# Kernel optimization log

Hardware: AMD Instinct MI355X
Metric: run time of the kernel (lower is better)

Reference implementation:

```python
import jax, jax.numpy as jnp
from jax import lax
import numpy as np

N_VOX = 50000
B = 2
D, H, W = 8, 160, 160
CIN = 16
G = 3
K = 27
CHANS = [(16, 16), (16, 32), (32, 64), (64, 64), (64, 128)]
NAMES = ['in', 'e1', 'e2', 'e3', 'out']


def setup_inputs() -> dict:
    key = jax.random.key(0)
    ks = jax.random.split(key, 16)
    rng = np.random.default_rng(0)
    # unique active cells -> deterministic scatter/gather rulebook
    lin = rng.choice(B * D * H * W, size=N_VOX, replace=False)
    bz = lin // (D * H * W)
    rem = lin % (D * H * W)
    zz = rem // (H * W)
    yy = (rem % (H * W)) // W
    xx = rem % W
    coors = jnp.asarray(np.stack([bz, zz, yy, xx], 1).astype(np.int32))
    inp = {
        'voxel_features': jax.random.normal(ks[0], (N_VOX, CIN), jnp.float32),
        'coors': coors,
        'batch_size': B,
    }
    i = 1
    for nm, (ci, co) in zip(NAMES, CHANS):
        k1, k2 = jax.random.split(ks[i]); i += 1
        inp['wb_' + nm] = jax.random.normal(k1, (K, ci, co), jnp.float32) * 0.05
        inp['ws_' + nm] = jax.random.normal(k2, (K, ci, G, co), jnp.float32) * 0.05
        inp['gm_' + nm] = jnp.ones((co,), jnp.float32)
        inp['bt_' + nm] = jnp.zeros((co,), jnp.float32)
    return inp


def _kan_block(feat, nbr, wb, ws, gm, bt, centers, inv_h):
    # submanifold KAN conv: gather -> (silu base + RBF spline basis) GEMM -> accumulate
    n = feat.shape[0]
    fp = jnp.concatenate([feat, jnp.zeros((1, feat.shape[1]), feat.dtype)], 0)  # pad row for out-of-grid

    def body(acc, kin):
        idx, wbk, wsk = kin
        x = fp[idx]                                   # [N, Cin] gathered neighbors
        base = jax.nn.silu(x) @ wbk                   # [N, Cout]
        bas = jnp.exp(-jnp.square((x[:, :, None] - centers) * inv_h))  # [N, Cin, G]
        spl = jnp.einsum('ncg,cgo->no', bas, wsk)     # [N, Cout]
        return acc + base + spl, None

    out0 = jnp.zeros((n, wb.shape[-1]), feat.dtype)
    out, _ = lax.scan(jax.checkpoint(body), out0, (nbr, wb, ws))
    # BatchNorm1d (train-mode batch stats) + ReLU
    mu = out.mean(0)
    var = out.var(0)
    out = (out - mu) * lax.rsqrt(var + 1e-3) * gm + bt
    return jax.nn.relu(out)


def _build_rulebook(coors, batch_size, n):
    grid = jnp.full((batch_size, D + 2, H + 2, W + 2), n, jnp.int32)
    grid = grid.at[coors[:, 0], coors[:, 1] + 1, coors[:, 2] + 1, coors[:, 3] + 1].set(
        jnp.arange(n, dtype=jnp.int32))
    offs = [(dz, dy, dx) for dz in (-1, 0, 1) for dy in (-1, 0, 1) for dx in (-1, 0, 1)]
    return jnp.stack([
        grid[coors[:, 0], coors[:, 1] + 1 + dz, coors[:, 2] + 1 + dy, coors[:, 3] + 1 + dx]
        for dz, dy, dx in offs])  # [27, N]


def reference(voxel_features, coors, batch_size,
              wb_in, ws_in, gm_in, bt_in,
              wb_e1, ws_e1, gm_e1, bt_e1,
              wb_e2, ws_e2, gm_e2, bt_e2,
              wb_e3, ws_e3, gm_e3, bt_e3,
              wb_out, ws_out, gm_out, bt_out):
    n = voxel_features.shape[0]
    nbr = _build_rulebook(coors, batch_size, n)
    centers = jnp.linspace(-1.0, 1.0, G)
    inv_h = (G - 1) / 2.0
    x = _kan_block(voxel_features, nbr, wb_in, ws_in, gm_in, bt_in, centers, inv_h)
    x = _kan_block(x, nbr, wb_e1, ws_e1, gm_e1, bt_e1, centers, inv_h)
    x = _kan_block(x, nbr, wb_e2, ws_e2, gm_e2, bt_e2, centers, inv_h)
    x = _kan_block(x, nbr, wb_e3, ws_e3, gm_e3, bt_e3, centers, inv_h)
    x = _kan_block(x, nbr, wb_out, ws_out, gm_out, bt_out, centers, inv_h)
    co = x.shape[1]
    dense = jnp.zeros((batch_size, D, H, W, co), x.dtype)
    dense = dense.at[coors[:, 0], coors[:, 1], coors[:, 2], coors[:, 3]].set(x)
    dense = dense.transpose(0, 4, 1, 2, 3)            # [B, C, D, H, W]
    return dense.reshape(batch_size, co * D, H, W)    # [B, C*D, H, W]
```

## Files before the change

### kernel.cpp

```cpp
#include <hip/hip_runtime.h>

#define N_VOX 50000
#define BATCH 2
#define DD 8
#define HH 160
#define WW 160
#define PD 10
#define PH 162
#define PW 162
#define KK 27
#define NCELL (BATCH*DD*HH*WW)
#define GRID_ELEMS (BATCH*PD*PH*PW)
#define OUT_ELEMS (BATCH*128*DD*HH*WW)

typedef __attribute__((ext_vector_type(8))) short short8v;
typedef __attribute__((ext_vector_type(4))) float float4v;

__device__ inline unsigned short f2bf(float f) {
    unsigned u = __float_as_uint(f);
    u += 0x7FFFu + ((u >> 16) & 1u);
    return (unsigned short)(u >> 16);
}

__device__ inline void gload_lds16(const void* g, void* l) {
    __builtin_amdgcn_global_load_lds(
        (const __attribute__((address_space(1))) void*)g,
        (__attribute__((address_space(3))) void*)l, 16, 0, 0);
}

__global__ void k_flags(const int* __restrict__ coors, int* __restrict__ flags) {
    int n = blockIdx.x * 256 + threadIdx.x;
    if (n >= N_VOX) return;
    int b = coors[n*4+0], z = coors[n*4+1], y = coors[n*4+2], x = coors[n*4+3];
    flags[((b*DD + z)*HH + y)*WW + x] = 1;
}

__global__ void k_scan1(const int* __restrict__ flags, int* __restrict__ scanout,
                        int* __restrict__ bsums) {
    __shared__ int s[256];
    int t = threadIdx.x, blk = blockIdx.x;
    int4 v = ((const int4*)(flags + blk*1024))[t];
    int tsum = v.x + v.y + v.z + v.w;
    s[t] = tsum; __syncthreads();
    for (int off = 1; off < 256; off <<= 1) {
        int x = (t >= off) ? s[t-off] : 0;
        __syncthreads(); s[t] += x; __syncthreads();
    }
    int excl = s[t] - tsum;
    int4 o; o.x = excl; o.y = excl + v.x; o.z = o.y + v.y; o.w = o.z + v.z;
    ((int4*)(scanout + blk*1024))[t] = o;
    if (t == 255) bsums[blk] = s[255];
}

__global__ void k_scan2(int* __restrict__ bsums) {
    __shared__ int s[512];
    int t = threadIdx.x;
    int orig = (t < 400) ? bsums[t] : 0;
    s[t] = orig; __syncthreads();
    for (int off = 1; off < 512; off <<= 1) {
        int x = (t >= off) ? s[t-off] : 0;
        __syncthreads(); s[t] += x; __syncthreads();
    }
    if (t < 400) bsums[t] = s[t] - orig;
}

__global__ void k_pos(const int* __restrict__ coors, const int* __restrict__ scanout,
                      const int* __restrict__ bsums, int* __restrict__ pos_of,
                      int* __restrict__ vox_at) {
    int n = blockIdx.x * 256 + threadIdx.x;
    if (n >= N_VOX) return;
    int b = coors[n*4+0], z = coors[n*4+1], y = coors[n*4+2], x = coors[n*4+3];
    int lin = ((b*DD + z)*HH + y)*WW + x;
    int pos = scanout[lin] + bsums[lin >> 10];
    pos_of[n] = pos;
    vox_at[pos] = n;
}

__global__ void k_gridP(const int* __restrict__ coors, const int* __restrict__ pos_of,
                        int* __restrict__ gridP) {
    int n = blockIdx.x * 256 + threadIdx.x;
    if (n >= N_VOX) return;
    int b = coors[n*4+0], z = coors[n*4+1], y = coors[n*4+2], x = coors[n*4+3];
    gridP[((b*PD + z+1)*PH + (y+1))*PW + (x+1)] = pos_of[n];
}

__global__ void k_nbrP(const int* __restrict__ coors, const int* __restrict__ vox_at,
                       const int* __restrict__ gridP, int* __restrict__ nbrP) {
    int i = blockIdx.x * 256 + threadIdx.x;
    if (i >= N_VOX) return;
    int n = vox_at[i];
    int b = coors[n*4+0], z = coors[n*4+1]+1, y = coors[n*4+2]+1, x = coors[n*4+3]+1;
    int k = 0;
    for (int dz = -1; dz <= 1; ++dz)
        for (int dy = -1; dy <= 1; ++dy)
            for (int dx = -1; dx <= 1; ++dx) {
                int g = gridP[((b*PD + z+dz)*PH + (y+dy))*PW + (x+dx)];
                nbrP[k*N_VOX + i] = (g >= 0) ? g : N_VOX;
                ++k;
            }
}

__global__ void k_phi0(const float* __restrict__ vf, const int* __restrict__ vox_at,
                       unsigned short* __restrict__ phi) {
    int e = blockIdx.x * 256 + threadIdx.x;
    if (e >= (N_VOX + 1) * 16) return;
    int i = e / 16, c = e % 16;
    float x = 0.f;
    if (i < N_VOX) x = vf[(size_t)vox_at[i] * 16 + c];
    float sig = 1.f / (1.f + __expf(-x));
    ushort4 p;
    p.x = f2bf(x * sig);
    p.y = f2bf(__expf(-(x + 1.f) * (x + 1.f)));
    p.z = f2bf(__expf(-x * x));
    p.w = f2bf(__expf(-(x - 1.f) * (x - 1.f)));
    *(ushort4*)&phi[(size_t)e * 4] = p;
}

struct WswzArgs {
    const float* wb[5];
    const float* ws[5];
    unsigned short* dst[5];
};
__global__ void k_wswz_all(WswzArgs a) {
    constexpr int off[6]   = {0, 27648, 82944, 304128, 746496, 1631232};
    constexpr int lgCI4[5] = {6, 6, 7, 8, 8};
    constexpr int lgCO[5]  = {4, 5, 6, 6, 7};
    int e = blockIdx.x * 256 + threadIdx.x;
    if (e >= off[5]) return;
    int L = 0;
    #pragma unroll
    for (int i = 1; i < 5; ++i) L += (e >= off[i]);
    int el = e - off[L];
    int CIN4 = 1 << lgCI4[L], COUT = 1 << lgCO[L], CIN = CIN4 >> 2;
    int j8   = el & 7;
    int rest = el >> 3;
    int o    = rest & (COUT - 1);
    int kb   = rest >> lgCO[L];
    int kabs = kb * 8 + j8;
    int k  = kabs >> lgCI4[L];
    int c4 = kabs & (CIN4 - 1);
    int c = c4 >> 2, jj = c4 & 3;
    float v = (jj == 0) ? a.wb[L][(k * CIN + c) * COUT + o]
                        : a.ws[L][((k * CIN + c) * 3 + (jj - 1)) * COUT + o];
    a.dst[L][el] = f2bf(v);
}

template<int CIN, int COUT, int NSPL>
__global__ __launch_bounds__(64, 2) void k_conv_mfma(
    const unsigned short* __restrict__ phi,
    const int*            __restrict__ nbrP,
    const unsigned short* __restrict__ Wsw,
    float*                __restrict__ pre,
    float*                __restrict__ sums)
{
    constexpr int CIN4   = CIN * 4;
    constexpr int BK     = 64;
    constexpr int SPK    = CIN4 / BK;
    constexpr int NSTAGE = KK * SPK;
    constexpr int COUTH  = COUT / NSPL;
    constexpr int NFW    = COUTH / 16;
    constexpr int WR     = 4;
    constexpr int NMB    = (N_VOX + 63) / 64;
    constexpr int NBLK   = NMB * NSPL;
    constexpr int PERX   = (NBLK + 7) / 8;

    int lb = blockIdx.x;
    int linear = (lb & 7) * PERX + (lb >> 3);
    if (linear >= NBLK) return;
    const int mb = linear / NSPL, h = linear % NSPL;

    const int lane = threadIdx.x & 63;
    const int l15 = lane & 15, q = lane >> 4;
    const int base = mb * 64;
    int vg[WR];
    #pragma unroll
    for (int rs = 0; rs < WR; ++rs) vg[rs] = base + rs * 16 + l15;
    const int ob = h * COUTH;

    const unsigned short* bp = Wsw + (size_t)(q * COUT + ob + l15) * 8;

    int rows[WR], rowsN[WR];
    short8v A0[2][WR], A1[2][WR];
    short8v B0[2][NFW], B1[2][NFW];

    auto loadB = [&](int sp, short8v (&Bb)[2][NFW]) {
        #pragma unroll
        for (int kk = 0; kk < 2; ++kk)
            #pragma unroll
            for (int nf = 0; nf < NFW; ++nf)
                Bb[kk][nf] = *(const short8v*)(bp +
                    ((size_t)(sp * 8 + kk * 4) * COUT + nf * 16) * 8);
    };
    auto loadA = [&](int sp, short8v (&Ab)[2][WR]) {
        if (sp % SPK == 0) {
            #pragma unroll
            for (int rs = 0; rs < WR; ++rs) rows[rs] = rowsN[rs];
        }
        const int c4s = (sp % SPK) * BK;
        #pragma unroll
        for (int rs = 0; rs < WR; ++rs) {
            const unsigned short* p = phi + (size_t)rows[rs] * CIN4 + c4s + q * 8;
            Ab[0][rs] = *(const short8v*)p;
            Ab[1][rs] = *(const short8v*)(p + 32);
        }
        if (sp % SPK == 0) {
            int k2 = sp / SPK + 1;
            if (k2 < KK) {
                #pragma unroll
                for (int rs = 0; rs < WR; ++rs)
                    rowsN[rs] = (vg[rs] < N_VOX) ? nbrP[k2 * N_VOX + vg[rs]] : N_VOX;
            }
        }
    };

    float4v acc[WR][NFW];
    #pragma unroll
    for (int rs = 0; rs < WR; ++rs)
        #pragma unroll
        for (int nf = 0; nf < NFW; ++nf)
            acc[rs][nf] = (float4v){0.f, 0.f, 0.f, 0.f};

    auto domfma = [&](const short8v (&Ab)[2][WR], const short8v (&Bb)[2][NFW]) {
        #pragma unroll
        for (int kk = 0; kk < 2; ++kk)
            #pragma unroll
            for (int nf = 0; nf < NFW; ++nf)
                #pragma unroll
                for (int rs = 0; rs < WR; ++rs)
                    acc[rs][nf] = __builtin_amdgcn_mfma_f32_16x16x32_bf16(
                        Ab[kk][rs], Bb[kk][nf], acc[rs][nf], 0, 0, 0);
    };

    #pragma unroll
    for (int rs = 0; rs < WR; ++rs) {
        rows[rs]  = (vg[rs] < N_VOX) ? nbrP[vg[rs]] : N_VOX;
        rowsN[rs] = (vg[rs] < N_VOX) ? nbrP[N_VOX + vg[rs]] : N_VOX;
    }
    loadB(0, B0);
    #pragma unroll
    for (int rs = 0; rs < WR; ++rs) {
        const unsigned short* p = phi + (size_t)rows[rs] * CIN4 + q * 8;
        A0[0][rs] = *(const short8v*)p;
        A0[1][rs] = *(const short8v*)(p + 32);
    }

    #define SLOT(T, Ac, Bc, An, Bn)                                   \
        if ((T) + 1 < NSTAGE) { loadB((T) + 1, Bn); loadA((T) + 1, An); } \
        __builtin_amdgcn_sched_barrier(0);                            \
        domfma(Ac, Bc);

    int s = 0;
    for (; s + 2 <= NSTAGE; s += 2) {
        SLOT(s + 0, A0, B0, A1, B1)
        SLOT(s + 1, A1, B1, A0, B0)
    }
    if constexpr (NSTAGE % 2 != 0) {
        domfma(A0, B0);
    }
    #undef SLOT

    #pragma unroll
    for (int rs = 0; rs < WR; ++rs)
        #pragma unroll
        for (int nf = 0; nf < NFW; ++nf)
            #pragma unroll
            for (int r = 0; r < 4; ++r) {
                int v = base + rs * 16 + q * 4 + r;
                if (v < N_VOX)
                    pre[(size_t)v * COUT + ob + nf * 16 + l15] = acc[rs][nf][r];
            }

    float* S = sums + (blockIdx.x & 7) * 256;
    #pragma unroll
    for (int nf = 0; nf < NFW; ++nf) {
        float s1 = 0.f, s2 = 0.f;
        #pragma unroll
        for (int rs = 0; rs < WR; ++rs)
            #pragma unroll
            for (int r = 0; r < 4; ++r) {
                int v = base + rs * 16 + q * 4 + r;
                if (v < N_VOX) {
                    float a = acc[rs][nf][r];
                    s1 += a; s2 += a * a;
                }
            }
        s1 += __shfl_xor(s1, 16); s1 += __shfl_xor(s1, 32);
        s2 += __shfl_xor(s2, 16); s2 += __shfl_xor(s2, 32);
        if (q == 0) {
            atomicAdd(&S[ob + nf * 16 + l15], s1);
            atomicAdd(&S[COUT + ob + nf * 16 + l15], s2);
        }
    }
}

template<int CIN, int COUT, int NSPL>
__global__ __launch_bounds__(256, 2) void k_conv_bsh(
    const unsigned short* __restrict__ phi,
    const int*            __restrict__ nbrP,
    const unsigned short* __restrict__ Wsw,
    float*                __restrict__ pre,
    float*                __restrict__ sums)
{
    constexpr int CIN4   = CIN * 4;
    constexpr int BK     = 64;
    constexpr int SPK    = CIN4 / BK;
    constexpr int NSTAGE = KK * SPK;
    constexpr int KB_G   = 8 * SPK;
    constexpr int COUTH  = COUT / NSPL;
    constexpr int NFW    = COUTH / 16;
    constexpr int WR     = 2;
    constexpr int NMB    = (N_VOX + 127) / 128;
    constexpr int NBLK   = NMB * NSPL;
    constexpr int PERX   = (NBLK + 7) / 8;
    constexpr int SI     = 2 * SPK;
    constexpr int VMCG   = 4 * SPK + 2;

    __shared__ short8v ldsB[2][KB_G][64];

    int lb = blockIdx.x;
    int linear = (lb & 7) * PERX + (lb >> 3);
    if (linear >= NBLK) return;
    const int mb = linear / NSPL, h = linear % NSPL;

    const int t = threadIdx.x, lane = t & 63, w = t >> 6;
    const int l15 = lane & 15, q = lane >> 4;
    const int base = mb * 128 + w * 32;
    int vg[WR];
    #pragma unroll
    for (int rs = 0; rs < WR; ++rs) vg[rs] = base + rs * 16 + l15;
    const int ob = h * COUTH;

    int rows[WR], rowsN[WR];
    short8v A0[2][WR], A1[2][WR];

    auto stage = [&](int g) {
        #pragma unroll
        for (int j = 0; j < SI; ++j) {
            const int m = w * SI + j;
            gload_lds16(Wsw + ((size_t)(g * KB_G + m) * COUT + ob + lane) * 8,
                        &ldsB[g & 1][m][0]);
        }
    };
    auto loadA = [&](int sp, short8v (&Ab)[2][WR]) {
        if (sp % SPK == 0) {
            #pragma unroll
            for (int rs = 0; rs < WR; ++rs) rows[rs] = rowsN[rs];
        }
        const int c4s = (sp % SPK) * BK;
        #pragma unroll
        for (int rs = 0; rs < WR; ++rs) {
            const unsigned short* p = phi + (size_t)rows[rs] * CIN4 + c4s + q * 8;
            Ab[0][rs] = *(const short8v*)p;
            Ab[1][rs] = *(const short8v*)(p + 32);
        }
        if (sp % SPK == 0) {
            int k2 = sp / SPK + 1;
            if (k2 < KK) {
                #pragma unroll
                for (int rs = 0; rs < WR; ++rs)
                    rowsN[rs] = (vg[rs] < N_VOX) ? nbrP[k2 * N_VOX + vg[rs]] : N_VOX;
            }
        }
    };

    float4v acc[WR][NFW];
    #pragma unroll
    for (int rs = 0; rs < WR; ++rs)
        #pragma unroll
        for (int nf = 0; nf < NFW; ++nf)
            acc[rs][nf] = (float4v){0.f, 0.f, 0.f, 0.f};

    stage(0);
    __builtin_amdgcn_sched_barrier(0);
    #pragma unroll
    for (int rs = 0; rs < WR; ++rs) {
        rows[rs]  = (vg[rs] < N_VOX) ? nbrP[vg[rs]] : N_VOX;
        rowsN[rs] = (vg[rs] < N_VOX) ? nbrP[N_VOX + vg[rs]] : N_VOX;
    }
    #pragma unroll
    for (int rs = 0; rs < WR; ++rs) {
        const unsigned short* p = phi + (size_t)rows[rs] * CIN4 + q * 8;
        A0[0][rs] = *(const short8v*)p;
        A0[1][rs] = *(const short8v*)(p + 32);
    }

    int sp = 0;
    #define SLOTB(SG, Ac, An)                                                 \
    {                                                                         \
        short8v bf[2][NFW];                                                   \
        _Pragma("unroll") for (int kk = 0; kk < 2; ++kk)                      \
        _Pragma("unroll") for (int nf = 0; nf < NFW; ++nf)                    \
            bf[kk][nf] = ldsB[g & 1][(SG) * 8 + kk * 4 + q][nf * 16 + l15];   \
        if (sp + 1 < NSTAGE) loadA(sp + 1, An);                               \
        __builtin_amdgcn_sched_barrier(0);                                    \
        _Pragma("unroll") for (int kk = 0; kk < 2; ++kk)                      \
        _Pragma("unroll") for (int nf = 0; nf < NFW; ++nf)                    \
        _Pragma("unroll") for (int rs = 0; rs < WR; ++rs)                     \
            acc[rs][nf] = __builtin_amdgcn_mfma_f32_16x16x32_bf16(            \
                Ac[kk][rs], bf[kk][nf], acc[rs][nf], 0, 0, 0);                \
        ++sp;                                                                 \
    }

    for (int g = 0; g < KK; ++g) {
        if (g == 0) { asm volatile("s_waitcnt vmcnt(8)" ::: "memory"); }
        else        { asm volatile("s_waitcnt vmcnt(%0)" :: "i"(VMCG) : "memory"); }
        __builtin_amdgcn_sched_barrier(0);
        __builtin_amdgcn_s_barrier();
        __builtin_amdgcn_sched_barrier(0);
        if (g + 1 < KK) stage(g + 1);
        __builtin_amdgcn_sched_barrier(0);
        SLOTB(0, A0, A1)
        SLOTB(1, A1, A0)
        if constexpr (SPK == 4) {
            SLOTB(2, A0, A1)
            SLOTB(3, A1, A0)
        }
    }
    #undef SLOTB

    #pragma unroll
    for (int rs = 0; rs < WR; ++rs)
        #pragma unroll
        for (int nf = 0; nf < NFW; ++nf)
            #pragma unroll
            for (int r = 0; r < 4; ++r) {
                int v = base + rs * 16 + q * 4 + r;
                if (v < N_VOX)
                    pre[(size_t)v * COUT + ob + nf * 16 + l15] = acc[rs][nf][r];
            }

    float* S = sums + (blockIdx.x & 7) * 256;
    #pragma unroll
    for (int nf = 0; nf < NFW; ++nf) {
        float s1 = 0.f, s2 = 0.f;
        #pragma unroll
        for (int rs = 0; rs < WR; ++rs)
            #pragma unroll
            for (int r = 0; r < 4; ++r) {
                int v = base + rs * 16 + q * 4 + r;
                if (v < N_VOX) {
                    float a = acc[rs][nf][r];
                    s1 += a; s2 += a * a;
                }
            }
        s1 += __shfl_xor(s1, 16); s1 += __shfl_xor(s1, 32);
        s2 += __shfl_xor(s2, 16); s2 += __shfl_xor(s2, 32);
        if (q == 0) {
            atomicAdd(&S[ob + nf * 16 + l15], s1);
            atomicAdd(&S[COUT + ob + nf * 16 + l15], s2);
        }
    }
}

template<int COUT>
__global__ void k_bnapply_phi(const float* __restrict__ pre, const float* __restrict__ sums,
                              const float* __restrict__ gm, const float* __restrict__ bt,
                              unsigned short* __restrict__ phi) {
    __shared__ float sc[COUT], sh[COUT];
    int t = threadIdx.x;
    if (t < COUT) {
        float s1 = 0.f, s2 = 0.f;
        #pragma unroll
        for (int xo = 0; xo < 8; ++xo) {
            s1 += sums[xo * 256 + t];
            s2 += sums[xo * 256 + COUT + t];
        }
        float mu  = s1 * (1.f / N_VOX);
        float var = s2 * (1.f / N_VOX) - mu*mu;
        float s = rsqrtf(var + 1e-3f) * gm[t];
        sc[t] = s;
        sh[t] = bt[t] - mu * s;
    }
    __syncthreads();
    int tot = (N_VOX + 1) * COUT;
    for (int e = blockIdx.x*256 + t; e < tot; e += gridDim.x*256) {
        int i = e / COUT, c = e % COUT;
        float x = 0.f;
        if (i < N_VOX) x = fmaxf(pre[(size_t)i*COUT + c] * sc[c] + sh[c], 0.f);
        float sig = 1.f / (1.f + __expf(-x));
        ushort4 p;
        p.x = f2bf(x * sig);
        p.y = f2bf(__expf(-(x + 1.f) * (x + 1.f)));
        p.z = f2bf(__expf(-x * x));
        p.w = f2bf(__expf(-(x - 1.f) * (x - 1.f)));
        *(ushort4*)&phi[(size_t)e * 4] = p;
    }
}

template<int COUT>
__global__ void k_bnapply_f32(float* __restrict__ pre, const float* __restrict__ sums,
                              const float* __restrict__ gm, const float* __restrict__ bt) {
    __shared__ float sc[COUT], sh[COUT];
    int t = threadIdx.x;
    if (t < COUT) {
        float s1 = 0.f, s2 = 0.f;
        #pragma unroll
        for (int xo = 0; xo < 8; ++xo) {
            s1 += sums[xo * 256 + t];
            s2 += sums[xo * 256 + COUT + t];
        }
        float mu  = s1 * (1.f / N_VOX);
        float var = s2 * (1.f / N_VOX) - mu*mu;
        float s = rsqrtf(var + 1e-3f) * gm[t];
        sc[t] = s;
        sh[t] = bt[t] - mu * s;
    }
    __syncthreads();
    for (int e = blockIdx.x*256 + t; e < N_VOX*COUT; e += gridDim.x*256) {
        int c = e % COUT;
        pre[e] = fmaxf(pre[e] * sc[c] + sh[c], 0.f);
    }
}

__global__ void k_dense(const float* __restrict__ feat, const int* __restrict__ gridP,
                        float* __restrict__ out) {
    int e4 = blockIdx.x*256 + threadIdx.x;
    if (e4 >= OUT_ELEMS/4) return;
    int e = e4 * 4;
    int x  = e % WW;
    int y  = (e / WW) % HH;
    int cz = (e / (WW*HH)) % (128*DD);
    int b  = e / (WW*HH*128*DD);
    int c = cz >> 3, z = cz & 7;
    const int* gp = &gridP[((b*PD + z+1)*PH + (y+1))*PW + (x+1)];
    int g0 = gp[0], g1 = gp[1], g2 = gp[2], g3 = gp[3];
    float4 o;
    o.x = (g0 >= 0) ? feat[(size_t)g0*128 + c] : 0.f;
    o.y = (g1 >= 0) ? feat[(size_t)g1*128 + c] : 0.f;
    o.z = (g2 >= 0) ? feat[(size_t)g2*128 + c] : 0.f;
    o.w = (g3 >= 0) ? feat[(size_t)g3*128 + c] : 0.f;
    *(float4*)&out[e] = o;
}

template<int CIN, int COUT, int NSPL>
static void run_block(const float* gm, const float* bt,
                      const int* nbrP, unsigned short* phi, const unsigned short* Wsw,
                      float* sums, float* pre, bool last, hipStream_t stream) {
    constexpr int NMB  = (N_VOX + 63) / 64;
    constexpr int NBLK = NMB * NSPL;
    constexpr int GRID = ((NBLK + 7) / 8) * 8;
    k_conv_mfma<CIN, COUT, NSPL><<<GRID, 64, 0, stream>>>(phi, nbrP, Wsw, pre, sums);
    if (last) {
        k_bnapply_f32<COUT><<<512, 256, 0, stream>>>(pre, sums, gm, bt);
    } else {
        k_bnapply_phi<COUT><<<512, 256, 0, stream>>>(pre, sums, gm, bt, phi);
    }
}

template<int CIN, int COUT, int NSPL>
static void run_block_bsh(const float* gm, const float* bt,
                          const int* nbrP, unsigned short* phi, const unsigned short* Wsw,
                          float* sums, float* pre, bool last, hipStream_t stream) {
    constexpr int NMB  = (N_VOX + 127) / 128;
    constexpr int NBLK = NMB * NSPL;
    constexpr int GRID = ((NBLK + 7) / 8) * 8;
    k_conv_bsh<CIN, COUT, NSPL><<<GRID, 256, 0, stream>>>(phi, nbrP, Wsw, pre, sums);
    if (last) {
        k_bnapply_f32<COUT><<<512, 256, 0, stream>>>(pre, sums, gm, bt);
    } else {
        k_bnapply_phi<COUT><<<512, 256, 0, stream>>>(pre, sums, gm, bt, phi);
    }
}

extern "C" void kernel_launch(void* const* d_in, const int* in_sizes, int n_in,
                              void* d_out, int out_size, void* d_ws, size_t ws_size,
                              hipStream_t stream) {
    const float* vf    = (const float*)d_in[0];
    const int*   coors = (const int*)d_in[1];
    const float* wb[5] = {(const float*)d_in[3],  (const float*)d_in[7],
                          (const float*)d_in[11], (const float*)d_in[15],
                          (const float*)d_in[19]};
    const float* wsp[5]= {(const float*)d_in[4],  (const float*)d_in[8],
                          (const float*)d_in[12], (const float*)d_in[16],
                          (const float*)d_in[20]};
    const float* gm[5] = {(const float*)d_in[5],  (const float*)d_in[9],
                          (const float*)d_in[13], (const float*)d_in[17],
                          (const float*)d_in[21]};
    const float* bt[5] = {(const float*)d_in[6],  (const float*)d_in[10],
                          (const float*)d_in[14], (const float*)d_in[18],
                          (const float*)d_in[22]};

    char* p = (char*)d_ws;
    auto alloc = [&](size_t bytes) {
        char* r = p;
        p += (bytes + 255) & ~(size_t)255;
        return r;
    };
    int*            flags   = (int*)           alloc((size_t)NCELL * 4);
    int*            scanout = (int*)           alloc((size_t)NCELL * 4);
    int*            bsums   = (int*)           alloc(512 * 4);
    int*            pos_of  = (int*)           alloc((size_t)N_VOX * 4);
    int*            vox_at  = (int*)           alloc((size_t)N_VOX * 4);
    int*            gridP   = (int*)           alloc((size_t)GRID_ELEMS * 4);
    int*            nbrP    = (int*)           alloc((size_t)KK * N_VOX * 4);
    unsigned short* Wsw0    = (unsigned short*)alloc((size_t)KK * 64  * 16  * 2);
    unsigned short* Wsw1    = (unsigned short*)alloc((size_t)KK * 64  * 32  * 2);
    unsigned short* Wsw2    = (unsigned short*)alloc((size_t)KK * 128 * 64  * 2);
    unsigned short* Wsw3    = (unsigned short*)alloc((size_t)KK * 256 * 64  * 2);
    unsigned short* Wsw4    = (unsigned short*)alloc((size_t)KK * 256 * 128 * 2);
    unsigned short* phi     = (unsigned short*)alloc((size_t)(N_VOX + 1) * 256 * 2);
    float*          sumsAll = (float*)         alloc(5 * 8 * 256 * 4);
    float*          pre     = (float*)         alloc((size_t)N_VOX * 128 * 4);

    hipMemsetAsync(flags, 0, (size_t)NCELL * 4, stream);
    hipMemsetAsync(gridP, 0xFF, (size_t)GRID_ELEMS * 4, stream);
    hipMemsetAsync(sumsAll, 0, 5 * 8 * 256 * 4, stream);

    WswzArgs wa;
    for (int i = 0; i < 5; ++i) { wa.wb[i] = wb[i]; wa.ws[i] = wsp[i]; }
    wa.dst[0] = Wsw0; wa.dst[1] = Wsw1; wa.dst[2] = Wsw2; wa.dst[3] = Wsw3; wa.dst[4] = Wsw4;
    k_wswz_all<<<(1631232 + 255) / 256, 256, 0, stream>>>(wa);

    k_flags<<<(N_VOX+255)/256, 256, 0, stream>>>(coors, flags);
    k_scan1<<<NCELL/1024, 256, 0, stream>>>(flags, scanout, bsums);
    k_scan2<<<1, 512, 0, stream>>>(bsums);
    k_pos  <<<(N_VOX+255)/256, 256, 0, stream>>>(coors, scanout, bsums, pos_of, vox_at);
    k_gridP<<<(N_VOX+255)/256, 256, 0, stream>>>(coors, pos_of, gridP);
    k_nbrP <<<(N_VOX+255)/256, 256, 0, stream>>>(coors, vox_at, gridP, nbrP);
    {
        int n = (N_VOX + 1) * 16;
        k_phi0<<<(n + 255) / 256, 256, 0, stream>>>(vf, vox_at, phi);
    }

    run_block<16, 16, 1>(gm[0], bt[0], nbrP, phi, Wsw0, sumsAll + 0*2048, pre, false, stream);
    run_block<16, 32, 1>(gm[1], bt[1], nbrP, phi, Wsw1, sumsAll + 1*2048, pre, false, stream);
    run_block_bsh<32, 64,  1>(gm[2], bt[2], nbrP, phi, Wsw2, sumsAll + 2*2048, pre, false, stream);
    run_block_bsh<64, 64,  1>(gm[3], bt[3], nbrP, phi, Wsw3, sumsAll + 3*2048, pre, false, stream);
    run_block_bsh<64, 128, 2>(gm[4], bt[4], nbrP, phi, Wsw4, sumsAll + 4*2048, pre, true,  stream);

    k_dense<<<(OUT_ELEMS/4 + 255)/256, 256, 0, stream>>>(pre, gridP, (float*)d_out);
}
```

Measured before the change: 633.5 us.

## Fuse final BN+ReLU into dense scatter and use 512-thread conv blocks

The last block's BatchNorm+ReLU pass over the f32 pre-activation buffer is removed. A tiny kernel now computes per-channel scale and shift, and the dense output kernel applies them while gathering. The bsh conv kernel also moves to 512-thread blocks covering 256 voxels, so each weight stage loaded into LDS is shared by twice as many voxels. The staging loads per warp drop and the vmcnt waits are adjusted, with a special case for the last stage. The larger blocks may reduce occupancy and leave fewer blocks to spread across the CUs.

New measurement: 629.5 us. About the same (-0.6%).

```diff
diff --git a/kernel.cpp b/kernel.cpp
--- a/kernel.cpp
+++ b/kernel.cpp
@@ -294,7 +294,7 @@
 }
 
 template<int CIN, int COUT, int NSPL>
-__global__ __launch_bounds__(256, 2) void k_conv_bsh(
+__global__ __launch_bounds__(512, 2) void k_conv_bsh(
     const unsigned short* __restrict__ phi,
     const int*            __restrict__ nbrP,
     const unsigned short* __restrict__ Wsw,
@@ -309,11 +309,10 @@
     constexpr int COUTH  = COUT / NSPL;
     constexpr int NFW    = COUTH / 16;
     constexpr int WR     = 2;
-    constexpr int NMB    = (N_VOX + 127) / 128;
+    constexpr int NMB    = (N_VOX + 255) / 256;
     constexpr int NBLK   = NMB * NSPL;
     constexpr int PERX   = (NBLK + 7) / 8;
-    constexpr int SI     = 2 * SPK;
-    constexpr int VMCG   = 4 * SPK + 2;
+    constexpr int SI     = KB_G / 8;
 
     __shared__ short8v ldsB[2][KB_G][64];
 
@@ -324,7 +323,7 @@
 
     const int t = threadIdx.x, lane = t & 63, w = t >> 6;
     const int l15 = lane & 15, q = lane >> 4;
-    const int base = mb * 128 + w * 32;
+    const int base = mb * 256 + w * 32;
     int vg[WR];
     #pragma unroll
     for (int rs = 0; rs < WR; ++rs) vg[rs] = base + rs * 16 + l15;
@@ -402,8 +401,13 @@
     }
 
     for (int g = 0; g < KK; ++g) {
-        if (g == 0) { asm volatile("s_waitcnt vmcnt(8)" ::: "memory"); }
-        else        { asm volatile("s_waitcnt vmcnt(%0)" :: "i"(VMCG) : "memory"); }
+        if (g == 0) {
+            asm volatile("s_waitcnt vmcnt(8)" ::: "memory");
+        } else if (g == KK - 1) {
+            asm volatile("s_waitcnt vmcnt(%0)" :: "i"(4 * SPK) : "memory");
+        } else {
+            asm volatile("s_waitcnt vmcnt(%0)" :: "i"(4 * SPK + 2) : "memory");
+        }
         __builtin_amdgcn_sched_barrier(0);
         __builtin_amdgcn_s_barrier();
         __builtin_amdgcn_sched_barrier(0);
@@ -487,33 +491,24 @@
     }
 }
 
-template<int COUT>
-__global__ void k_bnapply_f32(float* __restrict__ pre, const float* __restrict__ sums,
-                              const float* __restrict__ gm, const float* __restrict__ bt) {
-    __shared__ float sc[COUT], sh[COUT];
+__global__ void k_bnfin(const float* __restrict__ sums, const float* __restrict__ gm,
+                        const float* __restrict__ bt, float* __restrict__ scsh) {
     int t = threadIdx.x;
-    if (t < COUT) {
-        float s1 = 0.f, s2 = 0.f;
-        #pragma unroll
-        for (int xo = 0; xo < 8; ++xo) {
-            s1 += sums[xo * 256 + t];
-            s2 += sums[xo * 256 + COUT + t];
-        }
-        float mu  = s1 * (1.f / N_VOX);
-        float var = s2 * (1.f / N_VOX) - mu*mu;
-        float s = rsqrtf(var + 1e-3f) * gm[t];
-        sc[t] = s;
-        sh[t] = bt[t] - mu * s;
-    }
-    __syncthreads();
-    for (int e = blockIdx.x*256 + t; e < N_VOX*COUT; e += gridDim.x*256) {
-        int c = e % COUT;
-        pre[e] = fmaxf(pre[e] * sc[c] + sh[c], 0.f);
-    }
+    float s1 = 0.f, s2 = 0.f;
+    #pragma unroll
+    for (int xo = 0; xo < 8; ++xo) {
+        s1 += sums[xo * 256 + t];
+        s2 += sums[xo * 256 + 128 + t];
+    }
+    float mu  = s1 * (1.f / N_VOX);
+    float var = s2 * (1.f / N_VOX) - mu*mu;
+    float s = rsqrtf(var + 1e-3f) * gm[t];
+    scsh[t]       = s;
+    scsh[128 + t] = bt[t] - mu * s;
 }
 
 __global__ void k_dense(const float* __restrict__ feat, const int* __restrict__ gridP,
-                        float* __restrict__ out) {
+                        const float* __restrict__ scsh, float* __restrict__ out) {
     int e4 = blockIdx.x*256 + threadIdx.x;
     if (e4 >= OUT_ELEMS/4) return;
     int e = e4 * 4;
@@ -522,44 +517,38 @@
     int cz = (e / (WW*HH)) % (128*DD);
     int b  = e / (WW*HH*128*DD);
     int c = cz >> 3, z = cz & 7;
+    float sc = scsh[c], sh = scsh[128 + c];
     const int* gp = &gridP[((b*PD + z+1)*PH + (y+1))*PW + (x+1)];
     int g0 = gp[0], g1 = gp[1], g2 = gp[2], g3 = gp[3];
     float4 o;
-    o.x = (g0 >= 0) ? feat[(size_t)g0*128 + c] : 0.f;
-    o.y = (g1 >= 0) ? feat[(size_t)g1*128 + c] : 0.f;
-    o.z = (g2 >= 0) ? feat[(size_t)g2*128 + c] : 0.f;
-    o.w = (g3 >= 0) ? feat[(size_t)g3*128 + c] : 0.f;
+    o.x = (g0 >= 0) ? fmaxf(feat[(size_t)g0*128 + c] * sc + sh, 0.f) : 0.f;
+    o.y = (g1 >= 0) ? fmaxf(feat[(size_t)g1*128 + c] * sc + sh, 0.f) : 0.f;
+    o.z = (g2 >= 0) ? fmaxf(feat[(size_t)g2*128 + c] * sc + sh, 0.f) : 0.f;
+    o.w = (g3 >= 0) ? fmaxf(feat[(size_t)g3*128 + c] * sc + sh, 0.f) : 0.f;
     *(float4*)&out[e] = o;
 }
 
 template<int CIN, int COUT, int NSPL>
 static void run_block(const float* gm, const float* bt,
                       const int* nbrP, unsigned short* phi, const unsigned short* Wsw,
-                      float* sums, float* pre, bool last, hipStream_t stream) {
+                      float* sums, float* pre, hipStream_t stream) {
     constexpr int NMB  = (N_VOX + 63) / 64;
     constexpr int NBLK = NMB * NSPL;
     constexpr int GRID = ((NBLK + 7) / 8) * 8;
     k_conv_mfma<CIN, COUT, NSPL><<<GRID, 64, 0, stream>>>(phi, nbrP, Wsw, pre, sums);
-    if (last) {
-        k_bnapply_f32<COUT><<<512, 256, 0, stream>>>(pre, sums, gm, bt);
-    } else {
-        k_bnapply_phi<COUT><<<512, 256, 0, stream>>>(pre, sums, gm, bt, phi);
-    }
+    k_bnapply_phi<COUT><<<512, 256, 0, stream>>>(pre, sums, gm, bt, phi);
 }
 
 template<int CIN, int COUT, int NSPL>
 static void run_block_bsh(const float* gm, const float* bt,
                           const int* nbrP, unsigned short* phi, const unsigned short* Wsw,
                           float* sums, float* pre, bool last, hipStream_t stream) {
-    constexpr int NMB  = (N_VOX + 127) / 128;
+    constexpr int NMB  = (N_VOX + 255) / 256;
     constexpr int NBLK = NMB * NSPL;
     constexpr int GRID = ((NBLK + 7) / 8) * 8;
-    k_conv_bsh<CIN, COUT, NSPL><<<GRID, 256, 0, stream>>>(phi, nbrP, Wsw, pre, sums);
-    if (last) {
-        k_bnapply_f32<COUT><<<512, 256, 0, stream>>>(pre, sums, gm, bt);
-    } else {
+    k_conv_bsh<CIN, COUT, NSPL><<<GRID, 512, 0, stream>>>(phi, nbrP, Wsw, pre, sums);
+    if (!last)
         k_bnapply_phi<COUT><<<512, 256, 0, stream>>>(pre, sums, gm, bt, phi);
-    }
 }
 
 extern "C" void kernel_launch(void* const* d_in, const int* in_sizes, int n_in,
@@ -601,6 +590,7 @@
     unsigned short* phi     = (unsigned short*)alloc((size_t)(N_VOX + 1) * 256 * 2);
     float*          sumsAll = (float*)         alloc(5 * 8 * 256 * 4);
     float*          pre     = (float*)         alloc((size_t)N_VOX * 128 * 4);
+    float*          scsh    = (float*)         alloc(256 * 4);
 
     hipMemsetAsync(flags, 0, (size_t)NCELL * 4, stream);
     hipMemsetAsync(gridP, 0xFF, (size_t)GRID_ELEMS * 4, stream);
@@ -622,11 +612,12 @@
         k_phi0<<<(n + 255) / 256, 256, 0, stream>>>(vf, vox_at, phi);
     }
 
-    run_block<16, 16, 1>(gm[0], bt[0], nbrP, phi, Wsw0, sumsAll + 0*2048, pre, false, stream);
-    run_block<16, 32, 1>(gm[1], bt[1], nbrP, phi, Wsw1, sumsAll + 1*2048, pre, false, stream);
+    run_block<16, 16, 1>(gm[0], bt[0], nbrP, phi, Wsw0, sumsAll + 0*2048, pre, stream);
+    run_block<16, 32, 1>(gm[1], bt[1], nbrP, phi, Wsw1, sumsAll + 1*2048, pre, stream);
     run_block_bsh<32, 64,  1>(gm[2], bt[2], nbrP, phi, Wsw2, sumsAll + 2*2048, pre, false, stream);
     run_block_bsh<64, 64,  1>(gm[3], bt[3], nbrP, phi, Wsw3, sumsAll + 3*2048, pre, false, stream);
     run_block_bsh<64, 128, 2>(gm[4], bt[4], nbrP, phi, Wsw4, sumsAll + 4*2048, pre, true,  stream);
 
-    k_dense<<<(OUT_ELEMS/4 + 255)/256, 256, 0, stream>>>(pre, gridP, (float*)d_out);
-}
+    k_bnfin<<<1, 128, 0, stream>>>(sumsAll + 4*2048, gm[4], bt[4], scsh);
+    k_dense<<<(OUT_ELEMS/4 + 255)/256, 256, 0, stream>>>(pre, gridP, scsh, (float*)d_out);
+}
```
